# Optimization experiments

Hardware: AMD Instinct MI355X
Metric: run time of the kernel (lower is better)

Reference implementation:

```python
import jax, jax.numpy as jnp
import numpy as np
from jax import lax

# Quantization / conv config (mirrors QuantizedConv2d init args)
INPUT_ZP = -3
OUTPUT_ZP = 5
INPUT_SCALE = 0.05
OUTPUT_SCALE = 0.1
STRIDE = 1
PAD = (1, 1)   # (pad_h, pad_w)
DILATION = 1
GROUPS = 1
FEATURE_BITWIDTH = 8
QMIN = -(1 << (FEATURE_BITWIDTH - 1))          # -128
QMAX = (1 << (FEATURE_BITWIDTH - 1)) - 1       # 127

N, CIN, H, W = 32, 128, 56, 56
COUT, KH, KW = 256, 3, 3


def setup_inputs() -> dict:
    key = jax.random.key(0)
    k1, k2, k3, k4 = jax.random.split(key, 4)
    # int8-range quantized input / weight (stored as int32 arrays)
    x = jax.random.randint(k1, (N, CIN, H, W), 0, 256, dtype=jnp.int32) - 128
    weight = jax.random.randint(k2, (COUT, CIN, KH, KW), 0, 128, dtype=jnp.int32) - 64
    bias = jax.random.randint(k3, (COUT,), -32, 32, dtype=jnp.int32)
    # per-output-channel weight scale, shape [COUT,1,1] so it broadcasts over NCHW
    weight_scale = jax.random.uniform(k4, (COUT, 1, 1), dtype=jnp.float32) * 0.01 + 1e-4
    return {"x": x, "weight": weight, "bias": bias, "weight_scale": weight_scale}


def reference(x, weight, bias, weight_scale):
    ph, pw = PAD
    # Pad with the input zero point (quantized-domain padding)
    x_f = jnp.pad(x.astype(jnp.float32), ((0, 0), (0, 0), (ph, ph), (pw, pw)),
                  constant_values=float(INPUT_ZP))
    w_f = weight.astype(jnp.float32)
    b_f = bias.astype(jnp.float32)[None, :, None, None]
    # float32 conv (GPU path of the original), padding already applied
    acc = lax.conv_general_dilated(
        x_f, w_f,
        window_strides=(STRIDE, STRIDE),
        padding='VALID',
        rhs_dilation=(DILATION, DILATION),
        feature_group_count=GROUPS,
        dimension_numbers=('NCHW', 'OIHW', 'NCHW'))
    # original: conv2d(..., bias=q_bias) then round -> int32, then bias added AGAIN
    out = jnp.round(acc + b_f).astype(jnp.int32)
    out = out + bias[None, :, None, None]
    # dequant -> requant epilogue with per-channel weight scale
    out = (out.astype(jnp.float32) * INPUT_SCALE * weight_scale[None]
           / OUTPUT_SCALE + OUTPUT_ZP)
    out = jnp.clip(jnp.round(out), QMIN, QMAX).astype(jnp.int8)
    return out
```

## Files before the change

### kernel.cpp

```cpp
#include <hip/hip_runtime.h>


typedef __attribute__((ext_vector_type(4))) int i32x4;

#define NB_N 32
#define CIN 128
#define HH 56
#define WW 56
#define PH 58
#define COUT 256
#define PIX_PER_IMG (HH*WW)
#define X_IMG_INTS (PIX_PER_IMG*CIN)
#define XP_ROW_BYTES (PH*CIN)
#define XP_IMG_BYTES (PH*XP_ROW_BYTES)
#define XQ_PAD_BYTES ((size_t)NB_N*XP_IMG_BYTES)
#define A_BYTES (6*XP_ROW_BYTES)

__global__ __launch_bounds__(256) void halo_kernel(signed char* __restrict__ xq) {
    const i32x4 pad = {(int)0xFDFDFDFD, (int)0xFDFDFDFD, (int)0xFDFDFDFD, (int)0xFDFDFDFD};
    signed char* img = xq + (size_t)blockIdx.x * XP_IMG_BYTES;
    for (int t = threadIdx.x; t < 928; t += 256) {
        int r = (t < 464) ? 0 : 57;
        int off = ((t < 464) ? t : t - 464) * 16;
        *(i32x4*)(img + (size_t)r * XP_ROW_BYTES + off) = pad;
    }
    for (int t = threadIdx.x; t < 896; t += 256) {
        int px = t >> 3;
        int q = t & 7;
        int r = 1 + (px >> 1);
        int w = (px & 1) ? 57 : 0;
        *(i32x4*)(img + ((size_t)r * PH + w) * CIN + q * 16) = pad;
    }
}

#define WPR 33
__global__ __launch_bounds__(256) void pack_x_kernel(const int* __restrict__ x,
                                                     signed char* __restrict__ xq) {
    __shared__ int tile[WW * WPR];
    int nh = blockIdx.x;
    int n = nh / HH, h = nh - n * HH;
    const int* src = x + (size_t)n * X_IMG_INTS + h * WW;
    int q = threadIdx.x & 15;
    int cg4 = threadIdx.x >> 4;
    if (q < 14) {
#pragma unroll
        for (int i = 0; i < 2; ++i) {
            int cg = cg4 + i * 16;
            i32x4 v0 = *(const i32x4*)(src + (cg * 4 + 0) * PIX_PER_IMG + q * 4);
            i32x4 v1 = *(const i32x4*)(src + (cg * 4 + 1) * PIX_PER_IMG + q * 4);
            i32x4 v2 = *(const i32x4*)(src + (cg * 4 + 2) * PIX_PER_IMG + q * 4);
            i32x4 v3 = *(const i32x4*)(src + (cg * 4 + 3) * PIX_PER_IMG + q * 4);
#pragma unroll
            for (int j = 0; j < 4; ++j) {
                int word = (v0[j] & 255) | ((v1[j] & 255) << 8) |
                           ((v2[j] & 255) << 16) | (v3[j] << 24);
                tile[(q * 4 + j) * WPR + cg] = word;
            }
        }
    }
    __syncthreads();
    int* dst = (int*)(xq + (size_t)n * XP_IMG_BYTES + ((size_t)(h + 1) * PH + 1) * CIN);
#pragma unroll
    for (int i = 0; i < 7; ++i) {
        int t = i * 256 + threadIdx.x;
        int w = t >> 5, c4 = t & 31;
        dst[w * 32 + c4] = tile[w * WPR + c4];
    }
}

__global__ __launch_bounds__(256) void pack_w_kernel(const int* __restrict__ w,
                                                     signed char* __restrict__ wq) {
    int idx = blockIdx.x * 256 + threadIdx.x;
    if (idx >= 9 * 2 * 16 * 64) return;
    int lane = idx & 63;
    int fid = idx >> 6;
    int t = fid / 32;
    int rem = fid - t * 32;
    int kb = rem >> 4;
    int nf = rem & 15;
    int cout = nf * 16 + (lane & 15);
    int cinb = kb * 64 + (lane >> 4) * 16;
    int kh = t / 3, kw = t - kh * 3;
    union { signed char b[16]; i32x4 v; } u;
#pragma unroll
    for (int j = 0; j < 16; ++j) {
        int cin = cinb + j;
        u.b[j] = (signed char)w[((cout * CIN + cin) * 3 + kh) * 3 + kw];
    }
    *(i32x4*)(wq + (size_t)idx * 16) = u.v;
}

__global__ __launch_bounds__(256, 3) void conv_kernel(const signed char* __restrict__ xq,
                                                      const signed char* __restrict__ wq,
                                                      const int* __restrict__ bias,
                                                      const float* __restrict__ wscale,
                                                      int* __restrict__ out) {
    __shared__ __align__(16) signed char lds[A_BYTES];
    const int tid = threadIdx.x;
    const int lane = tid & 63, wv = tid >> 6;
    const int row = lane & 15, grp = lane >> 4;

    int orig = (blockIdx.x & 7) * 224 + (blockIdx.x >> 3);
    int n = orig / 56;
    int rr = orig - n * 56;
    int rb = rr >> 2;
    int cq = rr & 3;
    int pxhalf = wv >> 1, chalf = wv & 1;

    const signed char* ximg = xq + (size_t)n * XP_IMG_BYTES + (size_t)rb * 4 * XP_ROW_BYTES;

#pragma unroll
    for (int k = 0; k < 11; ++k) {
        int d = k * 4096 + tid * 16;
        if (d < A_BYTES) {
            int g = d ^ (((d >> 7) & 7) << 4);
            i32x4 v = *(const i32x4*)(ximg + g);
            *(i32x4*)(lds + d) = v;
        }
    }
    __syncthreads();

    int pc[7];
#pragma unroll
    for (int m = 0; m < 7; ++m) {
        int off = pxhalf * 112 + m * 16 + row;
        int lr = (off >= 56) + (off >= 112) + (off >= 168);
        int w = off - lr * 56;
        pc[m] = (lr + 1) * PH + (w + 1);
    }

    const int tapd[9] = {-PH - 1, -PH, -PH + 1, -1, 0, 1, PH - 1, PH, PH + 1};

    const signed char* wbase = wq + (size_t)(cq * 4 + chalf * 2) * 1024 + lane * 16;

    i32x4 acc[7][2] = {};
    i32x4 bn0 = *(const i32x4*)(wbase);
    i32x4 bn1 = *(const i32x4*)(wbase + 1024);

#pragma unroll
    for (int s = 0; s < 18; ++s) {
        const int t = s >> 1, kb = s & 1;
        i32x4 b0 = bn0, b1 = bn1;
        if (s < 17) {
            bn0 = *(const i32x4*)(wbase + (s + 1) * 16384);
            bn1 = *(const i32x4*)(wbase + (s + 1) * 16384 + 1024);
        }
        i32x4 a[7];
#pragma unroll
        for (int m = 0; m < 7; ++m) {
            int pix = pc[m] + tapd[t];
            int g = (pix << 7) + (kb << 6) + (grp << 4);
            int d = g ^ ((pix & 7) << 4);
            a[m] = *(const i32x4*)(lds + d);
        }
        __builtin_amdgcn_s_setprio(1);
#pragma unroll
        for (int m = 0; m < 7; ++m) {
            acc[m][0] = __builtin_amdgcn_mfma_i32_16x16x64_i8(a[m], b0, acc[m][0], 0, 0, 0);
            acc[m][1] = __builtin_amdgcn_mfma_i32_16x16x64_i8(a[m], b1, acc[m][1], 0, 0, 0);
        }
        __builtin_amdgcn_s_setprio(0);
    }

    float sc[2];
    int b2[2];
    const int coutbase = cq * 64 + chalf * 32;
#pragma unroll
    for (int j = 0; j < 2; ++j) {
        int cout = coutbase + j * 16 + row;
        sc[j] = wscale[cout] * 0.5f;
        b2[j] = 2 * bias[cout];
    }
    const int pixbase = rb * 224 + pxhalf * 112;
#pragma unroll
    for (int m = 0; m < 7; ++m) {
        int pl = pixbase + m * 16 + grp * 4;
        size_t obase = (size_t)n * (COUT * PIX_PER_IMG) + pl;
#pragma unroll
        for (int j = 0; j < 2; ++j) {
            int cout = coutbase + j * 16 + row;
            i32x4 v;
#pragma unroll
            for (int r = 0; r < 4; ++r) {
                int o = acc[m][j][r] + b2[j];
                float f = fmaf((float)o, sc[j], 5.0f);
                f = rintf(f);
                f = fminf(fmaxf(f, -128.0f), 127.0f);
                v[r] = (int)f;
            }
            *(i32x4*)(out + obase + (size_t)cout * PIX_PER_IMG) = v;
        }
    }
}

extern "C" void kernel_launch(void* const* d_in, const int* in_sizes, int n_in,
                              void* d_out, int out_size, void* d_ws, size_t ws_size,
                              hipStream_t stream) {
    const int* x = (const int*)d_in[0];
    const int* w = (const int*)d_in[1];
    const int* bias = (const int*)d_in[2];
    const float* ws = (const float*)d_in[3];
    int* out = (int*)d_out;

    signed char* xq = (signed char*)d_ws;
    signed char* wq = xq + XQ_PAD_BYTES;

    halo_kernel<<<NB_N, 256, 0, stream>>>(xq);
    pack_x_kernel<<<NB_N * HH, 256, 0, stream>>>(x, xq);
    pack_w_kernel<<<72, 256, 0, stream>>>(w, wq);
    conv_kernel<<<1792, 256, 0, stream>>>(xq, wq, bias, ws, out);
}
```

Before: 65.14 us.

## Fuse input int8 packing and halo padding into the conv kernel

Removes the separate halo and pack_x kernels and the padded int8 workspace. Each conv block now reads the int32 NCHW input directly, packs it into int8 channel-last form with the swizzled layout in LDS, and fills the padding with the zero-point byte itself. This saves two launches and a write/read round trip of the packed tensor. The cost is that each row band is converted 4 times (once per cout quarter), so int32 input traffic rises roughly fourfold. The s_setprio hints around the MFMA loop are also dropped.

```diff
diff --git a/kernel.cpp b/kernel.cpp
--- a/kernel.cpp
+++ b/kernel.cpp
@@ -11,62 +11,7 @@
 #define COUT 256
 #define PIX_PER_IMG (HH*WW)
 #define X_IMG_INTS (PIX_PER_IMG*CIN)
-#define XP_ROW_BYTES (PH*CIN)
-#define XP_IMG_BYTES (PH*XP_ROW_BYTES)
-#define XQ_PAD_BYTES ((size_t)NB_N*XP_IMG_BYTES)
-#define A_BYTES (6*XP_ROW_BYTES)
-
-__global__ __launch_bounds__(256) void halo_kernel(signed char* __restrict__ xq) {
-    const i32x4 pad = {(int)0xFDFDFDFD, (int)0xFDFDFDFD, (int)0xFDFDFDFD, (int)0xFDFDFDFD};
-    signed char* img = xq + (size_t)blockIdx.x * XP_IMG_BYTES;
-    for (int t = threadIdx.x; t < 928; t += 256) {
-        int r = (t < 464) ? 0 : 57;
-        int off = ((t < 464) ? t : t - 464) * 16;
-        *(i32x4*)(img + (size_t)r * XP_ROW_BYTES + off) = pad;
-    }
-    for (int t = threadIdx.x; t < 896; t += 256) {
-        int px = t >> 3;
-        int q = t & 7;
-        int r = 1 + (px >> 1);
-        int w = (px & 1) ? 57 : 0;
-        *(i32x4*)(img + ((size_t)r * PH + w) * CIN + q * 16) = pad;
-    }
-}
-
-#define WPR 33
-__global__ __launch_bounds__(256) void pack_x_kernel(const int* __restrict__ x,
-                                                     signed char* __restrict__ xq) {
-    __shared__ int tile[WW * WPR];
-    int nh = blockIdx.x;
-    int n = nh / HH, h = nh - n * HH;
-    const int* src = x + (size_t)n * X_IMG_INTS + h * WW;
-    int q = threadIdx.x & 15;
-    int cg4 = threadIdx.x >> 4;
-    if (q < 14) {
-#pragma unroll
-        for (int i = 0; i < 2; ++i) {
-            int cg = cg4 + i * 16;
-            i32x4 v0 = *(const i32x4*)(src + (cg * 4 + 0) * PIX_PER_IMG + q * 4);
-            i32x4 v1 = *(const i32x4*)(src + (cg * 4 + 1) * PIX_PER_IMG + q * 4);
-            i32x4 v2 = *(const i32x4*)(src + (cg * 4 + 2) * PIX_PER_IMG + q * 4);
-            i32x4 v3 = *(const i32x4*)(src + (cg * 4 + 3) * PIX_PER_IMG + q * 4);
-#pragma unroll
-            for (int j = 0; j < 4; ++j) {
-                int word = (v0[j] & 255) | ((v1[j] & 255) << 8) |
-                           ((v2[j] & 255) << 16) | (v3[j] << 24);
-                tile[(q * 4 + j) * WPR + cg] = word;
-            }
-        }
-    }
-    __syncthreads();
-    int* dst = (int*)(xq + (size_t)n * XP_IMG_BYTES + ((size_t)(h + 1) * PH + 1) * CIN);
-#pragma unroll
-    for (int i = 0; i < 7; ++i) {
-        int t = i * 256 + threadIdx.x;
-        int w = t >> 5, c4 = t & 31;
-        dst[w * 32 + c4] = tile[w * WPR + c4];
-    }
-}
+#define A_BYTES (6*PH*CIN)
 
 __global__ __launch_bounds__(256) void pack_w_kernel(const int* __restrict__ w,
                                                      signed char* __restrict__ wq) {
@@ -90,7 +35,7 @@
     *(i32x4*)(wq + (size_t)idx * 16) = u.v;
 }
 
-__global__ __launch_bounds__(256, 3) void conv_kernel(const signed char* __restrict__ xq,
+__global__ __launch_bounds__(256, 3) void conv_kernel(const int* __restrict__ x,
                                                       const signed char* __restrict__ wq,
                                                       const int* __restrict__ bias,
                                                       const float* __restrict__ wscale,
@@ -107,15 +52,44 @@
     int cq = rr & 3;
     int pxhalf = wv >> 1, chalf = wv & 1;
 
-    const signed char* ximg = xq + (size_t)n * XP_IMG_BYTES + (size_t)rb * 4 * XP_ROW_BYTES;
-
+    const int h0 = rb * 4 - 1;
+    for (int task = tid; task < 672; task += 256) {
+        int r = task / 112;
+        int rem = task - r * 112;
+        int wq4 = rem >> 3;
+        int co = rem & 7;
+        int h = h0 + r;
+        if ((unsigned)h < (unsigned)HH) {
+            const int* src = x + ((size_t)n * CIN + co * 16) * PIX_PER_IMG + h * WW + wq4 * 4;
+            int wds[4][4] = {{0,0,0,0},{0,0,0,0},{0,0,0,0},{0,0,0,0}};
 #pragma unroll
-    for (int k = 0; k < 11; ++k) {
-        int d = k * 4096 + tid * 16;
-        if (d < A_BYTES) {
-            int g = d ^ (((d >> 7) & 7) << 4);
-            i32x4 v = *(const i32x4*)(ximg + g);
-            *(i32x4*)(lds + d) = v;
+            for (int k = 0; k < 16; ++k) {
+                i32x4 v = *(const i32x4*)(src + k * PIX_PER_IMG);
+#pragma unroll
+                for (int j = 0; j < 4; ++j)
+                    wds[j][k >> 2] |= (v[j] & 255) << ((k & 3) * 8);
+            }
+#pragma unroll
+            for (int j = 0; j < 4; ++j) {
+                int pix = r * PH + (wq4 * 4 + j + 1);
+                int d = ((pix << 7) + co * 16) ^ ((pix & 7) << 4);
+                i32x4 wv4 = {wds[j][0], wds[j][1], wds[j][2], wds[j][3]};
+                *(i32x4*)(lds + d) = wv4;
+            }
+        }
+    }
+    {
+        const i32x4 pad = {(int)0xFDFDFDFD, (int)0xFDFDFDFD, (int)0xFDFDFDFD, (int)0xFDFDFDFD};
+        for (int t = tid; t < 6 * PH; t += 256) {
+            int r = t / PH, px = t - r * PH;
+            int h = h0 + r, w = px - 1;
+            if (!(((unsigned)h < (unsigned)HH) && ((unsigned)w < (unsigned)WW))) {
+#pragma unroll
+                for (int co = 0; co < 8; ++co) {
+                    int d = ((t << 7) + co * 16) ^ ((t & 7) << 4);
+                    *(i32x4*)(lds + d) = pad;
+                }
+            }
         }
     }
     __syncthreads();
@@ -153,13 +127,11 @@
             int d = g ^ ((pix & 7) << 4);
             a[m] = *(const i32x4*)(lds + d);
         }
-        __builtin_amdgcn_s_setprio(1);
 #pragma unroll
         for (int m = 0; m < 7; ++m) {
             acc[m][0] = __builtin_amdgcn_mfma_i32_16x16x64_i8(a[m], b0, acc[m][0], 0, 0, 0);
             acc[m][1] = __builtin_amdgcn_mfma_i32_16x16x64_i8(a[m], b1, acc[m][1], 0, 0, 0);
         }
-        __builtin_amdgcn_s_setprio(0);
     }
 
     float sc[2];
@@ -202,11 +174,8 @@
     const float* ws = (const float*)d_in[3];
     int* out = (int*)d_out;
 
-    signed char* xq = (signed char*)d_ws;
-    signed char* wq = xq + XQ_PAD_BYTES;
+    signed char* wq = (signed char*)d_ws;
 
-    halo_kernel<<<NB_N, 256, 0, stream>>>(xq);
-    pack_x_kernel<<<NB_N * HH, 256, 0, stream>>>(x, xq);
     pack_w_kernel<<<72, 256, 0, stream>>>(w, wq);
-    conv_kernel<<<1792, 256, 0, stream>>>(xq, wq, bias, ws, out);
+    conv_kernel<<<1792, 256, 0, stream>>>(x, wq, bias, ws, out);
 }
```

Measured after the change: 70.82 us. 1.09x slower.

## Fuse halo fill into pack_x and widen conv blocks to 512 threads

Applied to the files above, without the earlier changes.

The separate halo kernel is removed, and pack_x now writes the zero-point padding for its own row, plus the top and bottom rows when it handles the first or last image row. Conv blocks are doubled to 8 waves covering 128 output channels, so each LDS input tile is shared by twice as many channels and LDS loads per output fall. Bias and scale loads move ahead of the main loop, and the s_setprio hints are dropped. This saves a kernel launch and halves the redundant input staging, at the cost of fewer, larger blocks and different occupancy.

```diff
diff --git a/kernel.cpp b/kernel.cpp
--- a/kernel.cpp
+++ b/kernel.cpp
@@ -16,23 +16,6 @@
 #define XQ_PAD_BYTES ((size_t)NB_N*XP_IMG_BYTES)
 #define A_BYTES (6*XP_ROW_BYTES)
 
-__global__ __launch_bounds__(256) void halo_kernel(signed char* __restrict__ xq) {
-    const i32x4 pad = {(int)0xFDFDFDFD, (int)0xFDFDFDFD, (int)0xFDFDFDFD, (int)0xFDFDFDFD};
-    signed char* img = xq + (size_t)blockIdx.x * XP_IMG_BYTES;
-    for (int t = threadIdx.x; t < 928; t += 256) {
-        int r = (t < 464) ? 0 : 57;
-        int off = ((t < 464) ? t : t - 464) * 16;
-        *(i32x4*)(img + (size_t)r * XP_ROW_BYTES + off) = pad;
-    }
-    for (int t = threadIdx.x; t < 896; t += 256) {
-        int px = t >> 3;
-        int q = t & 7;
-        int r = 1 + (px >> 1);
-        int w = (px & 1) ? 57 : 0;
-        *(i32x4*)(img + ((size_t)r * PH + w) * CIN + q * 16) = pad;
-    }
-}
-
 #define WPR 33
 __global__ __launch_bounds__(256) void pack_x_kernel(const int* __restrict__ x,
                                                      signed char* __restrict__ xq) {
@@ -40,6 +23,7 @@
     int nh = blockIdx.x;
     int n = nh / HH, h = nh - n * HH;
     const int* src = x + (size_t)n * X_IMG_INTS + h * WW;
+    signed char* img = xq + (size_t)n * XP_IMG_BYTES;
     int q = threadIdx.x & 15;
     int cg4 = threadIdx.x >> 4;
     if (q < 14) {
@@ -58,8 +42,24 @@
             }
         }
     }
+    const i32x4 pad = {(int)0xFDFDFDFD, (int)0xFDFDFDFD, (int)0xFDFDFDFD, (int)0xFDFDFDFD};
+    {
+        int t = threadIdx.x;
+        if (t < 16) {
+            int w = (t >> 3) ? 57 : 0;
+            *(i32x4*)(img + ((size_t)(h + 1) * PH + w) * CIN + (t & 7) * 16) = pad;
+        }
+    }
+    if (h == 0) {
+        for (int t = threadIdx.x; t < 464; t += 256)
+            *(i32x4*)(img + (size_t)t * 16) = pad;
+    }
+    if (h == HH - 1) {
+        for (int t = threadIdx.x; t < 464; t += 256)
+            *(i32x4*)(img + (size_t)57 * XP_ROW_BYTES + t * 16) = pad;
+    }
     __syncthreads();
-    int* dst = (int*)(xq + (size_t)n * XP_IMG_BYTES + ((size_t)(h + 1) * PH + 1) * CIN);
+    int* dst = (int*)(img + ((size_t)(h + 1) * PH + 1) * CIN);
 #pragma unroll
     for (int i = 0; i < 7; ++i) {
         int t = i * 256 + threadIdx.x;
@@ -90,7 +90,7 @@
     *(i32x4*)(wq + (size_t)idx * 16) = u.v;
 }
 
-__global__ __launch_bounds__(256, 3) void conv_kernel(const signed char* __restrict__ xq,
+__global__ __launch_bounds__(512, 4) void conv_kernel(const signed char* __restrict__ xq,
                                                       const signed char* __restrict__ wq,
                                                       const int* __restrict__ bias,
                                                       const float* __restrict__ wscale,
@@ -100,24 +100,35 @@
     const int lane = tid & 63, wv = tid >> 6;
     const int row = lane & 15, grp = lane >> 4;
 
-    int orig = (blockIdx.x & 7) * 224 + (blockIdx.x >> 3);
-    int n = orig / 56;
-    int rr = orig - n * 56;
-    int rb = rr >> 2;
-    int cq = rr & 3;
-    int pxhalf = wv >> 1, chalf = wv & 1;
+    int orig = (blockIdx.x & 7) * 112 + (blockIdx.x >> 3);
+    int n = orig / 28;
+    int rr = orig - n * 28;
+    int rb = rr >> 1;
+    int cb = rr & 1;
+    int pxhalf = wv >> 2, cquad = wv & 3;
 
     const signed char* ximg = xq + (size_t)n * XP_IMG_BYTES + (size_t)rb * 4 * XP_ROW_BYTES;
 
 #pragma unroll
-    for (int k = 0; k < 11; ++k) {
-        int d = k * 4096 + tid * 16;
+    for (int k = 0; k < 6; ++k) {
+        int d = k * 8192 + tid * 16;
         if (d < A_BYTES) {
             int g = d ^ (((d >> 7) & 7) << 4);
             i32x4 v = *(const i32x4*)(ximg + g);
             *(i32x4*)(lds + d) = v;
         }
     }
+
+    float sc[2];
+    int b2[2];
+    const int coutbase = cb * 128 + cquad * 32;
+#pragma unroll
+    for (int j = 0; j < 2; ++j) {
+        int cout = coutbase + j * 16 + row;
+        sc[j] = wscale[cout] * 0.5f;
+        b2[j] = 2 * bias[cout];
+    }
+
     __syncthreads();
 
     int pc[7];
@@ -131,7 +142,7 @@
 
     const int tapd[9] = {-PH - 1, -PH, -PH + 1, -1, 0, 1, PH - 1, PH, PH + 1};
 
-    const signed char* wbase = wq + (size_t)(cq * 4 + chalf * 2) * 1024 + lane * 16;
+    const signed char* wbase = wq + (size_t)(cb * 8 + cquad * 2) * 1024 + lane * 16;
 
     i32x4 acc[7][2] = {};
     i32x4 bn0 = *(const i32x4*)(wbase);
@@ -153,24 +164,13 @@
             int d = g ^ ((pix & 7) << 4);
             a[m] = *(const i32x4*)(lds + d);
         }
-        __builtin_amdgcn_s_setprio(1);
 #pragma unroll
         for (int m = 0; m < 7; ++m) {
             acc[m][0] = __builtin_amdgcn_mfma_i32_16x16x64_i8(a[m], b0, acc[m][0], 0, 0, 0);
             acc[m][1] = __builtin_amdgcn_mfma_i32_16x16x64_i8(a[m], b1, acc[m][1], 0, 0, 0);
         }
-        __builtin_amdgcn_s_setprio(0);
-    }
-
-    float sc[2];
-    int b2[2];
-    const int coutbase = cq * 64 + chalf * 32;
-#pragma unroll
-    for (int j = 0; j < 2; ++j) {
-        int cout = coutbase + j * 16 + row;
-        sc[j] = wscale[cout] * 0.5f;
-        b2[j] = 2 * bias[cout];
-    }
+    }
+
     const int pixbase = rb * 224 + pxhalf * 112;
 #pragma unroll
     for (int m = 0; m < 7; ++m) {
@@ -205,8 +205,7 @@
     signed char* xq = (signed char*)d_ws;
     signed char* wq = xq + XQ_PAD_BYTES;
 
-    halo_kernel<<<NB_N, 256, 0, stream>>>(xq);
     pack_x_kernel<<<NB_N * HH, 256, 0, stream>>>(x, xq);
     pack_w_kernel<<<72, 256, 0, stream>>>(w, wq);
-    conv_kernel<<<1792, 256, 0, stream>>>(xq, wq, bias, ws, out);
-}
+    conv_kernel<<<896, 512, 0, stream>>>(xq, wq, bias, ws, out);
+}
```

New measurement: 73.86 us. +13.4%, slower.
